# Kernel tuning notes

Hardware: AMD Instinct MI355X
Metric: run time of the kernel (lower is better)

Reference implementation:

```python
import jax, jax.numpy as jnp
import numpy as np
from jax import lax

WS = 8          # window size
HEADS = 8
DIM = 192       # embed_dim == v_dim inside block
HD = DIM // HEADS
SCALE = HD ** -0.5
EPS = 1e-5


def _rel_pos_index(ws):
    coords = np.stack(np.meshgrid(np.arange(ws), np.arange(ws), indexing='ij'))  # (2,ws,ws)
    cf = coords.reshape(2, -1)                       # (2, n)
    rel = (cf[:, :, None] - cf[:, None, :]).transpose(1, 2, 0).astype(np.int64)  # (n,n,2)
    rel[..., 0] += ws - 1
    rel[..., 1] += ws - 1
    rel[..., 0] *= 2 * ws - 1
    return rel.sum(-1)                               # (n, n) int


def _ln(x, w, b):
    m = jnp.mean(x, axis=-1, keepdims=True)
    v = jnp.mean(jnp.square(x - m), axis=-1, keepdims=True)
    return (x - m) * lax.rsqrt(v + EPS) * w + b


def _conv3x3(x, w, b):
    y = lax.conv_general_dilated(x, w, (1, 1), ((1, 1), (1, 1)),
                                 dimension_numbers=('NCHW', 'OIHW', 'NCHW'))
    return y + b[None, :, None, None]


def setup_inputs():
    key = jax.random.key(0)
    ks = jax.random.split(key, 24)
    f = lambda k, shape: (jax.random.normal(k, shape, jnp.float32) * 0.02)
    inp = {
        'x': jax.random.normal(ks[0], (8, 96, 128, 128), jnp.float32),
        'v': jax.random.normal(ks[1], (8, 96, 128, 128), jnp.float32),
        'pq_w': f(ks[2], (DIM, 96, 3, 3)), 'pq_b': f(ks[3], (DIM,)),
        'pv_w': f(ks[4], (DIM, 96, 3, 3)), 'pv_b': f(ks[5], (DIM,)),
        'n1_w': jnp.ones((DIM,)), 'n1_b': jnp.zeros((DIM,)),
        'n2_w': jnp.ones((DIM,)), 'n2_b': jnp.zeros((DIM,)),
        'n3_w': jnp.ones((DIM,)), 'n3_b': jnp.zeros((DIM,)),
        'n4_w': jnp.ones((DIM,)), 'n4_b': jnp.zeros((DIM,)),
        'q_w': f(ks[6], (DIM, DIM)),
        'kv_w': f(ks[7], (2 * DIM, DIM)),
        'ap_w': f(ks[8], (DIM, DIM)), 'ap_b': f(ks[9], (DIM,)),
        'rpb': f(ks[10], ((2 * WS - 1) * (2 * WS - 1), HEADS)),
        'fc1_w': f(ks[11], (4 * DIM, DIM)), 'fc1_b': f(ks[12], (4 * DIM,)),
        'fc2_w': f(ks[13], (DIM, 4 * DIM)), 'fc2_b': f(ks[14], (DIM,)),
    }
    return inp


def reference(x, v, pq_w, pq_b, pv_w, pv_b, n1_w, n1_b, n2_w, n2_b, n3_w, n3_b,
              n4_w, n4_b, q_w, kv_w, ap_w, ap_b, rpb, fc1_w, fc1_b, fc2_w, fc2_b):
    # conv projections (input_dim != embed_dim, v_dim != embed_dim)
    x = _conv3x3(x, pq_w, pq_b)
    v = _conv3x3(v, pv_w, pv_b)
    x_proj, v_proj = x, v
    b, c, h, w = x.shape
    n = WS * WS

    xs = _ln(x.reshape(b, c, h * w).transpose(0, 2, 1), n1_w, n1_b).reshape(b, h, w, c)
    vs = _ln(v.reshape(b, c, h * w).transpose(0, 2, 1), n2_w, n2_b).reshape(b, h, w, c)

    pad_r = (WS - w % WS) % WS
    pad_b_ = (WS - h % WS) % WS
    if pad_r or pad_b_:
        xs = jnp.pad(xs, ((0, 0), (0, pad_b_), (0, pad_r), (0, 0)))
        vs = jnp.pad(vs, ((0, 0), (0, pad_b_), (0, pad_r), (0, 0)))
    hp, wp = h + pad_b_, w + pad_r

    def partition(t):  # (b,hp,wp,c) -> (nw, n, c)
        t = t.reshape(b, hp // WS, WS, wp // WS, WS, c)
        return t.transpose(0, 1, 3, 2, 4, 5).reshape(-1, n, c)

    xw = partition(xs)
    vw = partition(vs)

    # cross-window attention
    q = (xw @ q_w.T).reshape(-1, n, HEADS, HD).transpose(0, 2, 1, 3) * SCALE  # (nw,H,n,hd)
    kv = (vw @ kv_w.T).reshape(-1, n, 2, HEADS, HD).transpose(2, 0, 3, 1, 4)
    k, vv = kv[0], kv[1]                                                     # (nw,H,n,hd)
    attn = jnp.einsum('whqd,whkd->whqk', q, k)
    rel_idx = _rel_pos_index(WS)                                             # static (n,n)
    bias = rpb[rel_idx.reshape(-1)].reshape(n, n, HEADS).transpose(2, 0, 1)  # (H,n,n)
    attn = jax.nn.softmax(attn + bias[None], axis=-1)
    out = jnp.einsum('whqk,whkd->whqd', attn, vv).transpose(0, 2, 1, 3).reshape(-1, n, c)
    out = out @ ap_w.T + ap_b                                                # (nw,n,c)

    # window reverse + crop
    out = out.reshape(b, hp // WS, wp // WS, WS, WS, c).transpose(0, 1, 3, 2, 4, 5)
    out = out.reshape(b, hp, wp, c)[:, :h, :w, :].reshape(b, h * w, c)

    # mlp: note original does x = mlp(norm3(x)); x = x + drop_path(x) -> 2*mlp_out
    m = _ln(out, n3_w, n3_b)
    m = jax.nn.gelu(m @ fc1_w.T + fc1_b, approximate=False) @ fc2_w.T + fc2_b
    m = m + m
    m = _ln(m, n4_w, n4_b)
    m = m.reshape(b, h, w, c).transpose(0, 3, 1, 2)
    return m + x_proj + v_proj
```

## Files before the change

kernel.cpp:

```cpp
#include <hip/hip_runtime.h>
#include <hip/hip_bf16.h>
#include <math.h>

typedef _Float16 f16;
typedef _Float16 half8 __attribute__((ext_vector_type(8)));
typedef float f32x4 __attribute__((ext_vector_type(4)));

#define IMG 128
#define CIN 96
#define CH  192
#define SCALE_Q 0.2041241452319315f

__device__ __forceinline__ f32x4 mfma16(half8 a, half8 b, f32x4 c) {
  return __builtin_amdgcn_mfma_f32_16x16x32_f16(a, b, c, 0, 0, 0);
}

template <bool WH>
__device__ __forceinline__ half8 loadW(const void* W, int row, int k, int ldk) {
  if constexpr (WH) {
    return *(const half8*)((const f16*)W + (size_t)row * ldk + k);
  } else {
    const float* p = (const float*)W + (size_t)row * ldk + k;
    const float4 a = *(const float4*)p;
    const float4 b = *(const float4*)(p + 4);
    half8 h;
    h[0] = (f16)a.x; h[1] = (f16)a.y; h[2] = (f16)a.z; h[3] = (f16)a.w;
    h[4] = (f16)b.x; h[5] = (f16)b.y; h[6] = (f16)b.z; h[7] = (f16)b.w;
    return h;
  }
}

__device__ __forceinline__ float gelu(float x) {
  const float u = 0.70710678118654752f * x;
  const float a = fabsf(u);
  const float t = 1.0f / (1.0f + 0.3275911f * a);
  const float poly = t * (0.254829592f + t * (-0.284496736f +
                     t * (1.421413741f + t * (-1.453152027f + t * 1.061405429f))));
  float er = 1.0f - poly * __expf(-u * u);
  er = (u < 0.f) ? -er : er;
  return 0.5f * x * (1.0f + er);
}

__global__ __launch_bounds__(256) void reorder_w(
    const float* __restrict__ pq_w, const float* __restrict__ pv_w,
    const float* __restrict__ qW, const float* __restrict__ kvW,
    f16* __restrict__ Wr, f16* __restrict__ wq16) {
  const int i = blockIdx.x * 256 + threadIdx.x;
  if (i < 2 * 192 * 864) {
    const int which = i / (192 * 864);
    const int rem = i - which * (192 * 864);
    const int co = rem / 864;
    const int kk = rem - co * 864;
    const int s = kk / 96;
    const int ci = kk - s * 96;
    const float* src = which ? pv_w : pq_w;
    Wr[i] = (f16)src[co * 864 + ci * 9 + s];
  } else if (wq16) {
    const int j = i - 2 * 192 * 864;
    if (j < 110592)
      wq16[j] = (f16)(j < 36864 ? qW[j] : kvW[j - 36864]);
  }
}

__global__ __launch_bounds__(256) void reorder_w2(
    const float* __restrict__ apW, const float* __restrict__ w1,
    const float* __restrict__ w2, f16* __restrict__ dst) {
  const int i = blockIdx.x * 256 + threadIdx.x;
  if (i >= 331776) return;
  float v;
  if (i < 36864)       v = apW[i];
  else if (i < 184320) v = w1[i - 36864];
  else                 v = w2[i - 184320];
  dst[i] = (f16)v;
}

__global__ __launch_bounds__(256, 2) void conv3x3_mfma(
    const float* __restrict__ xin, const float* __restrict__ vin,
    const f16* __restrict__ Wr,
    const float* __restrict__ pq_b, const float* __restrict__ pv_b,
    f16* __restrict__ xp, f16* __restrict__ vp) {
  int bz = blockIdx.x;
  const int which = bz >> 10; bz &= 1023;
  const int b = bz >> 7;
  const int yp = (bz >> 1) & 63;
  const int xseg = bz & 1;
  const int y0 = yp * 2;
  const int x0 = xseg * 64;
  const float* in = which ? vin : xin;
  const float* bias = which ? pv_b : pq_b;
  const f16* W = Wr + (size_t)which * 192 * 864;
  f16* out = which ? vp : xp;

  __shared__ __align__(16) f16 ST[4 * 66 * 104];
  const int tid = threadIdx.x;
  #pragma unroll
  for (int batch = 0; batch < 9; ++batch) {
    float vals[11];
    bool oks[11];
    int sts[11];
    #pragma unroll
    for (int u = 0; u < 11; ++u) {
      const int i = tid + (batch * 11 + u) * 256;
      const int r = i / 6336;
      const int rem2 = i - r * 6336;
      const int c = rem2 / 66;
      const int xx = rem2 - c * 66;
      const int gy = y0 + r - 1;
      const int gx = x0 - 1 + xx;
      oks[u] = ((unsigned)gy < IMG) && ((unsigned)gx < IMG);
      const int cgy = min(max(gy, 0), IMG - 1);
      const int cgx = min(max(gx, 0), IMG - 1);
      vals[u] = in[(((size_t)b * CIN + c) * IMG + cgy) * IMG + cgx];
      sts[u] = (r * 66 + xx) * 104 + c;
    }
    #pragma unroll
    for (int u = 0; u < 11; ++u)
      ST[sts[u]] = oks[u] ? (f16)vals[u] : (f16)0.f;
  }
  __syncthreads();

  const int lane = tid & 63;
  const int wv = tid >> 6;
  const int l15 = lane & 15;
  const int quad = lane >> 4;
  const int nb = wv * 48;

  f32x4 acc[8][3];
  #pragma unroll
  for (int mt = 0; mt < 8; ++mt)
    #pragma unroll
    for (int j = 0; j < 3; ++j) acc[mt][j] = (f32x4)0.f;

  #pragma unroll
  for (int s = 0; s < 9; ++s) {
    const int ky = s / 3, kx = s - ky * 3;
    #pragma unroll
    for (int kstep = 0; kstep < 3; ++kstep) {
      const int k = kstep * 32 + quad * 8;
      half8 a[8];
      #pragma unroll
      for (int mt = 0; mt < 8; ++mt)
        a[mt] = *(const half8*)(ST + (((mt >> 2) + ky) * 66 + (mt & 3) * 16 + l15 + kx) * 104 + k);
      #pragma unroll
      for (int j = 0; j < 3; ++j) {
        const half8 bf = *(const half8*)(W + (size_t)(nb + j * 16 + l15) * 864 + s * 96 + k);
        #pragma unroll
        for (int mt = 0; mt < 8; ++mt) acc[mt][j] = mfma16(a[mt], bf, acc[mt][j]);
      }
    }
  }
  __syncthreads();

  #pragma unroll
  for (int j = 0; j < 3; ++j) {
    const int n = nb + j * 16 + l15;
    const float bn = bias[n];
    #pragma unroll
    for (int mt = 0; mt < 8; ++mt) {
      const int lt = (mt >> 2) * 64 + (mt & 3) * 16 + quad * 4;
      #pragma unroll
      for (int reg = 0; reg < 4; ++reg)
        ST[(lt + reg) * 204 + n] = (f16)(acc[mt][j][reg] + bn);
    }
  }
  __syncthreads();

  const size_t rowbase0 = ((size_t)(b * IMG + y0) * IMG + x0) * CH;
  const size_t rowbase1 = ((size_t)(b * IMG + y0 + 1) * IMG + x0) * CH;
  #pragma unroll
  for (int it = 0; it < 12; ++it) {
    const int i = tid + it * 256;
    const int tok = i / 24, c8 = i - tok * 24;
    const half8 hval = *(const half8*)(ST + tok * 204 + c8 * 8);
    const int trow = tok >> 6, tx = tok & 63;
    f16* dst = out + (trow ? rowbase1 : rowbase0) + (size_t)tx * CH + c8 * 8;
    *(half8*)dst = hval;
  }
}

template <bool WH>
__global__ __launch_bounds__(256, 1) void ln_qkv_mfma(
    f16* __restrict__ xp, const f16* __restrict__ vp,
    const float* __restrict__ n1w, const float* __restrict__ n1b,
    const float* __restrict__ n2w, const float* __restrict__ n2b,
    const void* __restrict__ qW, const void* __restrict__ kvW,
    f16* __restrict__ qb, f16* __restrict__ kb, f16* __restrict__ vb) {
  const int tid = threadIdx.x;
  const int lane = tid & 63;
  const int wv = tid >> 6;
  const int l15 = lane & 15;
  const int quad = lane >> 4;
  const int tok0 = blockIdx.x * 32;
  __shared__ __align__(16) f16 U[32 * 588];
  f16* Ax = U;
  f16* Av = U + 6400;

  {
    const int r = tid >> 3;
    const int s = tid & 7;
    const size_t gbase = (size_t)(tok0 + r) * 192 + s * 24;
    half8 hx[3], hv[3];
    const half8* px = (const half8*)(xp + gbase);
    const half8* pv = (const half8*)(vp + gbase);
    #pragma unroll
    for (int i = 0; i < 3; ++i) { hx[i] = px[i]; hv[i] = pv[i]; }
    float xv[24], vvv[24];
    float sx = 0.f, sx2 = 0.f, sv = 0.f, sv2 = 0.f;
    #pragma unroll
    for (int i = 0; i < 24; ++i) {
      xv[i] = (float)hx[i >> 3][i & 7];
      vvv[i] = (float)hv[i >> 3][i & 7];
      sx += xv[i]; sx2 += xv[i] * xv[i];
      sv += vvv[i]; sv2 += vvv[i] * vvv[i];
    }
    half8 hr[3];
    #pragma unroll
    for (int i = 0; i < 24; ++i) hr[i >> 3][i & 7] = (f16)(xv[i] + vvv[i]);
    half8* pr = (half8*)(xp + gbase);
    #pragma unroll
    for (int i = 0; i < 3; ++i) pr[i] = hr[i];
    #pragma unroll
    for (int m = 1; m < 8; m <<= 1) {
      sx += __shfl_xor(sx, m, 64); sx2 += __shfl_xor(sx2, m, 64);
      sv += __shfl_xor(sv, m, 64); sv2 += __shfl_xor(sv2, m, 64);
    }
    const float mx = sx * (1.f / 192.f);
    const float rx = rsqrtf(sx2 * (1.f / 192.f) - mx * mx + 1e-5f);
    const float mv = sv * (1.f / 192.f);
    const float rv = rsqrtf(sv2 * (1.f / 192.f) - mv * mv + 1e-5f);
    #pragma unroll
    for (int i = 0; i < 24; ++i) {
      const int c = s * 24 + i;
      Ax[r * 200 + c] = (f16)((xv[i] - mx) * rx * n1w[c] + n1b[c]);
      Av[r * 200 + c] = (f16)((vvv[i] - mv) * rv * n2w[c] + n2b[c]);
    }
  }
  __syncthreads();

  const int nb = wv * 144;
  f32x4 acc[2][9];
  #pragma unroll
  for (int mt = 0; mt < 2; ++mt)
    #pragma unroll
    for (int j = 0; j < 9; ++j) acc[mt][j] = (f32x4)0.f;

  for (int kc = 0; kc < 6; ++kc) {
    const int k = kc * 32 + quad * 8;
    half8 wb[9];
    #pragma unroll
    for (int j = 0; j < 9; ++j) {
      const int n0 = nb + j * 16;
      if (n0 < 192) wb[j] = loadW<WH>(qW, n0 + l15, k, 192);
      else          wb[j] = loadW<WH>(kvW, n0 - 192 + l15, k, 192);
    }
    const half8 ax0 = *(const half8*)(Ax + l15 * 200 + k);
    const half8 ax1 = *(const half8*)(Ax + (16 + l15) * 200 + k);
    const half8 av0 = *(const half8*)(Av + l15 * 200 + k);
    const half8 av1 = *(const half8*)(Av + (16 + l15) * 200 + k);
    #pragma unroll
    for (int j = 0; j < 9; ++j) {
      const int n0 = nb + j * 16;
      if (n0 < 192) {
        acc[0][j] = mfma16(ax0, wb[j], acc[0][j]);
        acc[1][j] = mfma16(ax1, wb[j], acc[1][j]);
      } else {
        acc[0][j] = mfma16(av0, wb[j], acc[0][j]);
        acc[1][j] = mfma16(av1, wb[j], acc[1][j]);
      }
    }
  }
  __syncthreads();

  #pragma unroll
  for (int j = 0; j < 9; ++j) {
    const int n = nb + j * 16 + l15;
    const float scale = (n < 192) ? SCALE_Q : 1.f;
    #pragma unroll
    for (int mt = 0; mt < 2; ++mt)
      #pragma unroll
      for (int reg = 0; reg < 4; ++reg) {
        const int r = mt * 16 + quad * 4 + reg;
        U[r * 588 + n] = (f16)(acc[mt][j][reg] * scale);
      }
  }
  __syncthreads();

  const int yrow = (tok0 >> 7) & 127;
  const int bb = tok0 >> 14;
  const int x0b = tok0 & 127;
  const int wib = bb * 256 + ((yrow >> 3) << 4) + (x0b >> 3);
  const int trow = (yrow & 7) * 8;
  f16* const bufs[3] = {qb, kb, vb};
  #pragma unroll
  for (int it = 0; it < 9; ++it) {
    const int i = tid + it * 256;
    const int c24 = i % 24;
    const int g = i / 24;
    const int h = g & 7;
    const int g2 = g >> 3;
    const int wloc = g2 & 3;
    const int buf = g2 >> 2;
    const int t8 = c24 / 3, c3 = c24 - t8 * 3;
    const int r = wloc * 8 + t8;
    const half8 hval = *(const half8*)(U + r * 588 + buf * 192 + h * 24 + c3 * 8);
    f16* dst = bufs[buf] + (size_t)(wib + wloc) * 12288 + (trow + t8) * 24 + h * 1536 + c3 * 8;
    *(half8*)dst = hval;
  }
}

__global__ __launch_bounds__(64) void attn64(
    const f16* __restrict__ qb, const f16* __restrict__ kb,
    const f16* __restrict__ vb, const float* __restrict__ rpb,
    f16* __restrict__ fb) {
  const int wh = blockIdx.x;
  const int h = wh & 7;
  const int w = wh >> 3;
  const int t = threadIdx.x;
  __shared__ __align__(16) float ks[64 * 24];
  __shared__ __align__(16) float vs[64 * 24];
  __shared__ float bsh[225];
  const f16* kbase = kb + (size_t)wh * 1536;
  const f16* vbase = vb + (size_t)wh * 1536;
  for (int i = t; i < 1536; i += 64) { ks[i] = (float)kbase[i]; vs[i] = (float)vbase[i]; }
  for (int i = t; i < 225; i += 64) bsh[i] = rpb[i * 8 + h];
  float q[24];
  const f16* qrow = qb + ((size_t)wh * 64 + t) * 24;
  #pragma unroll
  for (int d = 0; d < 24; ++d) q[d] = (float)qrow[d];
  __syncthreads();
  const int qy = t >> 3, qx = t & 7;
  float s[64];
  float mx = -1e30f;
  #pragma unroll
  for (int kk = 0; kk < 64; ++kk) {
    float acc = 0.f;
    #pragma unroll
    for (int d = 0; d < 24; ++d) acc += q[d] * ks[kk * 24 + d];
    const int ky = kk >> 3, kx = kk & 7;
    acc += bsh[(qy - ky + 7) * 15 + (qx - kx + 7)];
    s[kk] = acc;
    mx = fmaxf(mx, acc);
  }
  float sum = 0.f;
  #pragma unroll
  for (int kk = 0; kk < 64; ++kk) { const float e = __expf(s[kk] - mx); s[kk] = e; sum += e; }
  const float inv = 1.0f / sum;
  float o[24];
  #pragma unroll
  for (int d = 0; d < 24; ++d) o[d] = 0.f;
  #pragma unroll
  for (int kk = 0; kk < 64; ++kk) {
    const float p = s[kk];
    #pragma unroll
    for (int d = 0; d < 24; ++d) o[d] += p * vs[kk * 24 + d];
  }
  f16* orow = fb + ((size_t)w * 64 + t) * 192 + h * 24;
  #pragma unroll
  for (int d = 0; d < 24; ++d) orow[d] = (f16)(o[d] * inv);
}

__global__ __launch_bounds__(256, 1) void ap_ln3_mfma(
    f16* __restrict__ fb, const f16* __restrict__ apW,
    const float* __restrict__ apb,
    const float* __restrict__ n3w, const float* __restrict__ n3b) {
  const int tid = threadIdx.x;
  const int lane = tid & 63;
  const int wv = tid >> 6;
  const int l15 = lane & 15;
  const int quad = lane >> 4;
  const int wt0 = blockIdx.x * 64;
  __shared__ __align__(16) f16 As[64 * 200];
  __shared__ float rs[64], rq[64];
  if (tid < 64) { rs[tid] = 0.f; rq[tid] = 0.f; }
  for (int i = tid; i < 64 * 24; i += 256) {
    const int r = i / 24, s = i - r * 24;
    *(half8*)(As + r * 200 + s * 8) = *(const half8*)(fb + (size_t)(wt0 + r) * 192 + s * 8);
  }
  __syncthreads();

  const int nb = wv * 48;
  f32x4 acc[4][3];
  #pragma unroll
  for (int mt = 0; mt < 4; ++mt)
    #pragma unroll
    for (int j = 0; j < 3; ++j) acc[mt][j] = (f32x4)0.f;

  #pragma unroll
  for (int g = 0; g < 2; ++g) {
    half8 wb[3][3];
    #pragma unroll
    for (int u = 0; u < 3; ++u) {
      const int k = (g * 3 + u) * 32 + quad * 8;
      #pragma unroll
      for (int j = 0; j < 3; ++j)
        wb[u][j] = *(const half8*)(apW + (size_t)(nb + j * 16 + l15) * 192 + k);
    }
    #pragma unroll
    for (int u = 0; u < 3; ++u) {
      const int k = (g * 3 + u) * 32 + quad * 8;
      half8 a[4];
      #pragma unroll
      for (int mt = 0; mt < 4; ++mt)
        a[mt] = *(const half8*)(As + (mt * 16 + l15) * 200 + k);
      #pragma unroll
      for (int j = 0; j < 3; ++j)
        #pragma unroll
        for (int mt = 0; mt < 4; ++mt) acc[mt][j] = mfma16(a[mt], wb[u][j], acc[mt][j]);
    }
  }
  float bias[3];
  #pragma unroll
  for (int j = 0; j < 3; ++j) bias[j] = apb[nb + j * 16 + l15];
  #pragma unroll
  for (int mt = 0; mt < 4; ++mt)
    #pragma unroll
    for (int j = 0; j < 3; ++j)
      #pragma unroll
      for (int reg = 0; reg < 4; ++reg) acc[mt][j][reg] += bias[j];

  float ssum[16], ssq[16];
  #pragma unroll
  for (int mt = 0; mt < 4; ++mt)
    #pragma unroll
    for (int reg = 0; reg < 4; ++reg) {
      const int i = mt * 4 + reg;
      const float a0 = acc[mt][0][reg], a1 = acc[mt][1][reg], a2 = acc[mt][2][reg];
      ssum[i] = a0 + a1 + a2;
      ssq[i] = a0 * a0 + a1 * a1 + a2 * a2;
    }
  #pragma unroll
  for (int m = 1; m < 16; m <<= 1)
    #pragma unroll
    for (int i = 0; i < 16; ++i) {
      ssum[i] += __shfl_xor(ssum[i], m, 64);
      ssq[i] += __shfl_xor(ssq[i], m, 64);
    }
  if (l15 == 0) {
    #pragma unroll
    for (int mt = 0; mt < 4; ++mt)
      #pragma unroll
      for (int reg = 0; reg < 4; ++reg) {
        const int row = mt * 16 + quad * 4 + reg;
        atomicAdd(&rs[row], ssum[mt * 4 + reg]);
        atomicAdd(&rq[row], ssq[mt * 4 + reg]);
      }
  }
  __syncthreads();

  float w3[3], b3[3]; int cc[3];
  #pragma unroll
  for (int j = 0; j < 3; ++j) {
    cc[j] = nb + j * 16 + l15;
    w3[j] = n3w[cc[j]]; b3[j] = n3b[cc[j]];
  }
  #pragma unroll
  for (int mt = 0; mt < 4; ++mt)
    #pragma unroll
    for (int reg = 0; reg < 4; ++reg) {
      const int row = mt * 16 + quad * 4 + reg;
      const float mean = rs[row] * (1.f / 192.f);
      const float rstd = rsqrtf(rq[row] * (1.f / 192.f) - mean * mean + 1e-5f);
      #pragma unroll
      for (int j = 0; j < 3; ++j)
        fb[(size_t)(wt0 + row) * 192 + cc[j]] =
            (f16)((acc[mt][j][reg] - mean) * rstd * w3[j] + b3[j]);
    }
}

__global__ __launch_bounds__(256, 2) void mlp_mfma(
    const f16* __restrict__ m, const f16* __restrict__ w1,
    const float* __restrict__ b1, const f16* __restrict__ w2,
    const float* __restrict__ b2,
    const float* __restrict__ n4w, const float* __restrict__ n4b,
    const f16* __restrict__ res, float* __restrict__ out) {
  const int tid = threadIdx.x;
  const int lane = tid & 63;
  const int wv = tid >> 6;
  const int l15 = lane & 15;
  const int quad = lane >> 4;
  const int wt0 = blockIdx.x * 32;
  __shared__ __align__(16) f16 SB[32 * 776];
  __shared__ float rs[32], rq[32];
  if (tid < 32) { rs[tid] = 0.f; rq[tid] = 0.f; }
  for (int i = tid; i < 32 * 24; i += 256) {
    const int r = i / 24, s = i - r * 24;
    *(half8*)(SB + r * 200 + s * 8) = *(const half8*)(m + (size_t)(wt0 + r) * 192 + s * 8);
  }
  __syncthreads();

  const int nb1 = wv * 192;
  f32x4 acc1[2][12];
  #pragma unroll
  for (int mt = 0; mt < 2; ++mt)
    #pragma unroll
    for (int j = 0; j < 12; ++j) acc1[mt][j] = (f32x4)0.f;
  for (int kc = 0; kc < 6; ++kc) {
    const int k = kc * 32 + quad * 8;
    half8 wb[12];
    #pragma unroll
    for (int j = 0; j < 12; ++j)
      wb[j] = *(const half8*)(w1 + (size_t)(nb1 + j * 16 + l15) * 192 + k);
    const half8 a0 = *(const half8*)(SB + l15 * 200 + k);
    const half8 a1 = *(const half8*)(SB + (16 + l15) * 200 + k);
    #pragma unroll
    for (int j = 0; j < 12; ++j) {
      acc1[0][j] = mfma16(a0, wb[j], acc1[0][j]);
      acc1[1][j] = mfma16(a1, wb[j], acc1[1][j]);
    }
  }
  __syncthreads();
  #pragma unroll
  for (int j = 0; j < 12; ++j) {
    const int n = nb1 + j * 16 + l15;
    const float bj = b1[n];
    #pragma unroll
    for (int mt = 0; mt < 2; ++mt)
      #pragma unroll
      for (int reg = 0; reg < 4; ++reg) {
        const int row = mt * 16 + quad * 4 + reg;
        SB[row * 776 + n] = (f16)gelu(acc1[mt][j][reg] + bj);
      }
  }
  __syncthreads();

  const int nb2 = wv * 48;
  int cc[3];
  #pragma unroll
  for (int j = 0; j < 3; ++j) cc[j] = nb2 + j * 16 + l15;
  const int wi = wt0 >> 6;
  const int t_base = wt0 & 63;
  const int b_img = wi >> 8;
  const int wy = (wi >> 4) & 15;
  const int wx = wi & 15;
  float rr[2][3][4];
  #pragma unroll
  for (int mt = 0; mt < 2; ++mt) {
    const int t0 = t_base + mt * 16 + quad * 4;
    const int y = wy * 8 + (t0 >> 3);
    const int xx0 = wx * 8 + (t0 & 7);
    const size_t tokbase = ((size_t)(b_img * 128 + y)) * 128 + xx0;
    #pragma unroll
    for (int j = 0; j < 3; ++j)
      #pragma unroll
      for (int reg = 0; reg < 4; ++reg)
        rr[mt][j][reg] = (float)res[(tokbase + reg) * 192 + cc[j]];
  }

  f32x4 acc2[2][3];
  #pragma unroll
  for (int mt = 0; mt < 2; ++mt)
    #pragma unroll
    for (int j = 0; j < 3; ++j) acc2[mt][j] = (f32x4)0.f;
  for (int g = 0; g < 6; ++g) {
    half8 wb[4][3];
    #pragma unroll
    for (int u = 0; u < 4; ++u) {
      const int k = (g * 4 + u) * 32 + quad * 8;
      #pragma unroll
      for (int j = 0; j < 3; ++j)
        wb[u][j] = *(const half8*)(w2 + (size_t)(nb2 + j * 16 + l15) * 768 + k);
    }
    #pragma unroll
    for (int u = 0; u < 4; ++u) {
      const int k = (g * 4 + u) * 32 + quad * 8;
      const half8 a0 = *(const half8*)(SB + l15 * 776 + k);
      const half8 a1 = *(const half8*)(SB + (16 + l15) * 776 + k);
      #pragma unroll
      for (int j = 0; j < 3; ++j) {
        acc2[0][j] = mfma16(a0, wb[u][j], acc2[0][j]);
        acc2[1][j] = mfma16(a1, wb[u][j], acc2[1][j]);
      }
    }
  }
  float w4[3], b4[3];
  #pragma unroll
  for (int j = 0; j < 3; ++j) {
    const float bj = b2[cc[j]];
    w4[j] = n4w[cc[j]]; b4[j] = n4b[cc[j]];
    #pragma unroll
    for (int mt = 0; mt < 2; ++mt)
      #pragma unroll
      for (int reg = 0; reg < 4; ++reg)
        acc2[mt][j][reg] = 2.f * (acc2[mt][j][reg] + bj);
  }
  float ssum[8], ssq[8];
  #pragma unroll
  for (int mt = 0; mt < 2; ++mt)
    #pragma unroll
    for (int reg = 0; reg < 4; ++reg) {
      const int i = mt * 4 + reg;
      const float a0 = acc2[mt][0][reg], a1 = acc2[mt][1][reg], a2 = acc2[mt][2][reg];
      ssum[i] = a0 + a1 + a2;
      ssq[i] = a0 * a0 + a1 * a1 + a2 * a2;
    }
  #pragma unroll
  for (int mm = 1; mm < 16; mm <<= 1)
    #pragma unroll
    for (int i = 0; i < 8; ++i) {
      ssum[i] += __shfl_xor(ssum[i], mm, 64);
      ssq[i] += __shfl_xor(ssq[i], mm, 64);
    }
  if (l15 == 0) {
    #pragma unroll
    for (int mt = 0; mt < 2; ++mt)
      #pragma unroll
      for (int reg = 0; reg < 4; ++reg) {
        const int row = mt * 16 + quad * 4 + reg;
        atomicAdd(&rs[row], ssum[mt * 4 + reg]);
        atomicAdd(&rq[row], ssq[mt * 4 + reg]);
      }
  }
  __syncthreads();

  #pragma unroll
  for (int mt = 0; mt < 2; ++mt) {
    const int row0 = mt * 16 + quad * 4;
    const int t0 = t_base + row0;
    const int y = wy * 8 + (t0 >> 3);
    const int x0 = wx * 8 + (t0 & 7);
    float mean[4], rstd[4];
    #pragma unroll
    for (int reg = 0; reg < 4; ++reg) {
      const int row = row0 + reg;
      mean[reg] = rs[row] * (1.f / 192.f);
      rstd[reg] = rsqrtf(rq[row] * (1.f / 192.f) - mean[reg] * mean[reg] + 1e-5f);
    }
    #pragma unroll
    for (int j = 0; j < 3; ++j) {
      float4 o;
      float vals[4];
      #pragma unroll
      for (int reg = 0; reg < 4; ++reg)
        vals[reg] = (acc2[mt][j][reg] - mean[reg]) * rstd[reg] * w4[j] + b4[j] + rr[mt][j][reg];
      o.x = vals[0]; o.y = vals[1]; o.z = vals[2]; o.w = vals[3];
      float* dst = out + ((size_t)(b_img * 192 + cc[j])) * 16384 + (y * 128 + x0);
      *(float4*)dst = o;
    }
  }
}

extern "C" void kernel_launch(void* const* d_in, const int* in_sizes, int n_in,
                              void* d_out, int out_size, void* d_ws, size_t ws_size,
                              hipStream_t stream) {
  (void)in_sizes; (void)n_in; (void)out_size;
  const float* x    = (const float*)d_in[0];
  const float* v    = (const float*)d_in[1];
  const float* pq_w = (const float*)d_in[2];
  const float* pq_b = (const float*)d_in[3];
  const float* pv_w = (const float*)d_in[4];
  const float* pv_b = (const float*)d_in[5];
  const float* n1w  = (const float*)d_in[6];
  const float* n1b  = (const float*)d_in[7];
  const float* n2w  = (const float*)d_in[8];
  const float* n2b  = (const float*)d_in[9];
  const float* n3w  = (const float*)d_in[10];
  const float* n3b  = (const float*)d_in[11];
  const float* n4w  = (const float*)d_in[12];
  const float* n4b  = (const float*)d_in[13];
  const float* qW   = (const float*)d_in[14];
  const float* kvW  = (const float*)d_in[15];
  const float* apW  = (const float*)d_in[16];
  const float* apb  = (const float*)d_in[17];
  const float* rpb  = (const float*)d_in[18];
  const float* w1   = (const float*)d_in[19];
  const float* b1   = (const float*)d_in[20];
  const float* w2   = (const float*)d_in[21];
  const float* b2   = (const float*)d_in[22];
  float* out = (float*)d_out;

  const size_t HE = 25165824;
  f16* xp   = (f16*)d_ws;
  f16* vp   = xp + HE;
  f16* vvb  = vp + HE;
  f16* qb   = (f16*)d_out;
  f16* kb   = qb + HE;
  f16* fb   = vp;
  f16* Wr   = vvb;
  f16* wtail = vvb + HE;
  const bool big = ws_size >= (3 * HE + 110592) * sizeof(f16);

  reorder_w<<<big ? 1728 : 1296, 256, 0, stream>>>(pq_w, pv_w, qW, kvW, Wr,
                                                   big ? wtail : (f16*)nullptr);
  conv3x3_mfma<<<2048, 256, 0, stream>>>(x, v, Wr, pq_b, pv_b, xp, vp);
  if (big)
    ln_qkv_mfma<true><<<4096, 256, 0, stream>>>(xp, vp, n1w, n1b, n2w, n2b,
                                                wtail, wtail + 36864, qb, kb, vvb);
  else
    ln_qkv_mfma<false><<<4096, 256, 0, stream>>>(xp, vp, n1w, n1b, n2w, n2b,
                                                 qW, kvW, qb, kb, vvb);
  attn64<<<16384, 64, 0, stream>>>(qb, kb, vvb, rpb, fb);
  reorder_w2<<<1296, 256, 0, stream>>>(apW, w1, w2, vvb);
  ap_ln3_mfma<<<2048, 256, 0, stream>>>(fb, vvb, apb, n3w, n3b);
  mlp_mfma<<<4096, 256, 0, stream>>>(fb, vvb + 36864, b1, vvb + 184320, b2,
                                     n4w, n4b, xp, out);
}
```

Baseline: 1.050 ms.

## Fuse attention output projection and LayerNorm3 into the MLP kernel

Merges the separate ap_ln3 kernel into the MLP kernel. Each 32-token block now computes the output projection, bias and LN3 in registers and writes the normalized result straight into shared memory for fc1, instead of round-tripping through global memory and paying an extra launch. The MLP kernel now carries extra accumulators and bias registers, which may raise register pressure at two blocks per CU. The GELU reciprocal is also switched to the fast hardware rcp instruction.

```diff
diff --git a/kernel.cpp b/kernel.cpp
--- a/kernel.cpp
+++ b/kernel.cpp
@@ -33,7 +33,7 @@
 __device__ __forceinline__ float gelu(float x) {
   const float u = 0.70710678118654752f * x;
   const float a = fabsf(u);
-  const float t = 1.0f / (1.0f + 0.3275911f * a);
+  const float t = __builtin_amdgcn_rcpf(1.0f + 0.3275911f * a);
   const float poly = t * (0.254829592f + t * (-0.284496736f +
                      t * (1.421413741f + t * (-1.453152027f + t * 1.061405429f))));
   float er = 1.0f - poly * __expf(-u * u);
@@ -359,118 +359,12 @@
   for (int d = 0; d < 24; ++d) orow[d] = (f16)(o[d] * inv);
 }
 
-__global__ __launch_bounds__(256, 1) void ap_ln3_mfma(
-    f16* __restrict__ fb, const f16* __restrict__ apW,
+__global__ __launch_bounds__(256, 2) void ap_mlp_mfma(
+    const f16* __restrict__ fb, const f16* __restrict__ apW,
     const float* __restrict__ apb,
-    const float* __restrict__ n3w, const float* __restrict__ n3b) {
-  const int tid = threadIdx.x;
-  const int lane = tid & 63;
-  const int wv = tid >> 6;
-  const int l15 = lane & 15;
-  const int quad = lane >> 4;
-  const int wt0 = blockIdx.x * 64;
-  __shared__ __align__(16) f16 As[64 * 200];
-  __shared__ float rs[64], rq[64];
-  if (tid < 64) { rs[tid] = 0.f; rq[tid] = 0.f; }
-  for (int i = tid; i < 64 * 24; i += 256) {
-    const int r = i / 24, s = i - r * 24;
-    *(half8*)(As + r * 200 + s * 8) = *(const half8*)(fb + (size_t)(wt0 + r) * 192 + s * 8);
-  }
-  __syncthreads();
-
-  const int nb = wv * 48;
-  f32x4 acc[4][3];
-  #pragma unroll
-  for (int mt = 0; mt < 4; ++mt)
-    #pragma unroll
-    for (int j = 0; j < 3; ++j) acc[mt][j] = (f32x4)0.f;
-
-  #pragma unroll
-  for (int g = 0; g < 2; ++g) {
-    half8 wb[3][3];
-    #pragma unroll
-    for (int u = 0; u < 3; ++u) {
-      const int k = (g * 3 + u) * 32 + quad * 8;
-      #pragma unroll
-      for (int j = 0; j < 3; ++j)
-        wb[u][j] = *(const half8*)(apW + (size_t)(nb + j * 16 + l15) * 192 + k);
-    }
-    #pragma unroll
-    for (int u = 0; u < 3; ++u) {
-      const int k = (g * 3 + u) * 32 + quad * 8;
-      half8 a[4];
-      #pragma unroll
-      for (int mt = 0; mt < 4; ++mt)
-        a[mt] = *(const half8*)(As + (mt * 16 + l15) * 200 + k);
-      #pragma unroll
-      for (int j = 0; j < 3; ++j)
-        #pragma unroll
-        for (int mt = 0; mt < 4; ++mt) acc[mt][j] = mfma16(a[mt], wb[u][j], acc[mt][j]);
-    }
-  }
-  float bias[3];
-  #pragma unroll
-  for (int j = 0; j < 3; ++j) bias[j] = apb[nb + j * 16 + l15];
-  #pragma unroll
-  for (int mt = 0; mt < 4; ++mt)
-    #pragma unroll
-    for (int j = 0; j < 3; ++j)
-      #pragma unroll
-      for (int reg = 0; reg < 4; ++reg) acc[mt][j][reg] += bias[j];
-
-  float ssum[16], ssq[16];
-  #pragma unroll
-  for (int mt = 0; mt < 4; ++mt)
-    #pragma unroll
-    for (int reg = 0; reg < 4; ++reg) {
-      const int i = mt * 4 + reg;
-      const float a0 = acc[mt][0][reg], a1 = acc[mt][1][reg], a2 = acc[mt][2][reg];
-      ssum[i] = a0 + a1 + a2;
-      ssq[i] = a0 * a0 + a1 * a1 + a2 * a2;
-    }
-  #pragma unroll
-  for (int m = 1; m < 16; m <<= 1)
-    #pragma unroll
-    for (int i = 0; i < 16; ++i) {
-      ssum[i] += __shfl_xor(ssum[i], m, 64);
-      ssq[i] += __shfl_xor(ssq[i], m, 64);
-    }
-  if (l15 == 0) {
-    #pragma unroll
-    for (int mt = 0; mt < 4; ++mt)
-      #pragma unroll
-      for (int reg = 0; reg < 4; ++reg) {
-        const int row = mt * 16 + quad * 4 + reg;
-        atomicAdd(&rs[row], ssum[mt * 4 + reg]);
-        atomicAdd(&rq[row], ssq[mt * 4 + reg]);
-      }
-  }
-  __syncthreads();
-
-  float w3[3], b3[3]; int cc[3];
-  #pragma unroll
-  for (int j = 0; j < 3; ++j) {
-    cc[j] = nb + j * 16 + l15;
-    w3[j] = n3w[cc[j]]; b3[j] = n3b[cc[j]];
-  }
-  #pragma unroll
-  for (int mt = 0; mt < 4; ++mt)
-    #pragma unroll
-    for (int reg = 0; reg < 4; ++reg) {
-      const int row = mt * 16 + quad * 4 + reg;
-      const float mean = rs[row] * (1.f / 192.f);
-      const float rstd = rsqrtf(rq[row] * (1.f / 192.f) - mean * mean + 1e-5f);
-      #pragma unroll
-      for (int j = 0; j < 3; ++j)
-        fb[(size_t)(wt0 + row) * 192 + cc[j]] =
-            (f16)((acc[mt][j][reg] - mean) * rstd * w3[j] + b3[j]);
-    }
-}
-
-__global__ __launch_bounds__(256, 2) void mlp_mfma(
-    const f16* __restrict__ m, const f16* __restrict__ w1,
-    const float* __restrict__ b1, const f16* __restrict__ w2,
-    const float* __restrict__ b2,
+    const float* __restrict__ n3w, const float* __restrict__ n3b,
+    const f16* __restrict__ w1, const float* __restrict__ b1,
+    const f16* __restrict__ w2, const float* __restrict__ b2,
     const float* __restrict__ n4w, const float* __restrict__ n4b,
     const f16* __restrict__ res, float* __restrict__ out) {
   const int tid = threadIdx.x;
@@ -480,15 +374,103 @@
   const int quad = lane >> 4;
   const int wt0 = blockIdx.x * 32;
   __shared__ __align__(16) f16 SB[32 * 776];
-  __shared__ float rs[32], rq[32];
-  if (tid < 32) { rs[tid] = 0.f; rq[tid] = 0.f; }
+  __shared__ float rs3[32], rq3[32], rs4[32], rq4[32];
+  if (tid < 32) { rs3[tid] = 0.f; rq3[tid] = 0.f; rs4[tid] = 0.f; rq4[tid] = 0.f; }
   for (int i = tid; i < 32 * 24; i += 256) {
     const int r = i / 24, s = i - r * 24;
-    *(half8*)(SB + r * 200 + s * 8) = *(const half8*)(m + (size_t)(wt0 + r) * 192 + s * 8);
-  }
-  __syncthreads();
-
+    *(half8*)(SB + r * 200 + s * 8) = *(const half8*)(fb + (size_t)(wt0 + r) * 192 + s * 8);
+  }
+  __syncthreads();
+
+  const int nbp = wv * 48;
+  int cc[3]; float apbv[3], w3v[3], b3v[3];
+  #pragma unroll
+  for (int j = 0; j < 3; ++j) {
+    cc[j] = nbp + j * 16 + l15;
+    apbv[j] = apb[cc[j]]; w3v[j] = n3w[cc[j]]; b3v[j] = n3b[cc[j]];
+  }
   const int nb1 = wv * 192;
+  float b1v[12];
+  #pragma unroll
+  for (int j = 0; j < 12; ++j) b1v[j] = b1[nb1 + j * 16 + l15];
+
+  f32x4 accp[2][3];
+  #pragma unroll
+  for (int mt = 0; mt < 2; ++mt)
+    #pragma unroll
+    for (int j = 0; j < 3; ++j) accp[mt][j] = (f32x4)0.f;
+  #pragma unroll
+  for (int g = 0; g < 2; ++g) {
+    half8 wb[3][3];
+    #pragma unroll
+    for (int u = 0; u < 3; ++u) {
+      const int k = (g * 3 + u) * 32 + quad * 8;
+      #pragma unroll
+      for (int j = 0; j < 3; ++j)
+        wb[u][j] = *(const half8*)(apW + (size_t)cc[j] * 192 + k);
+    }
+    #pragma unroll
+    for (int u = 0; u < 3; ++u) {
+      const int k = (g * 3 + u) * 32 + quad * 8;
+      const half8 a0 = *(const half8*)(SB + l15 * 200 + k);
+      const half8 a1 = *(const half8*)(SB + (16 + l15) * 200 + k);
+      #pragma unroll
+      for (int j = 0; j < 3; ++j) {
+        accp[0][j] = mfma16(a0, wb[u][j], accp[0][j]);
+        accp[1][j] = mfma16(a1, wb[u][j], accp[1][j]);
+      }
+    }
+  }
+  #pragma unroll
+  for (int mt = 0; mt < 2; ++mt)
+    #pragma unroll
+    for (int j = 0; j < 3; ++j)
+      #pragma unroll
+      for (int reg = 0; reg < 4; ++reg) accp[mt][j][reg] += apbv[j];
+
+  {
+    float ssum[8], ssq[8];
+    #pragma unroll
+    for (int mt = 0; mt < 2; ++mt)
+      #pragma unroll
+      for (int reg = 0; reg < 4; ++reg) {
+        const int i = mt * 4 + reg;
+        const float a0 = accp[mt][0][reg], a1 = accp[mt][1][reg], a2 = accp[mt][2][reg];
+        ssum[i] = a0 + a1 + a2;
+        ssq[i] = a0 * a0 + a1 * a1 + a2 * a2;
+      }
+    #pragma unroll
+    for (int mm = 1; mm < 16; mm <<= 1)
+      #pragma unroll
+      for (int i = 0; i < 8; ++i) {
+        ssum[i] += __shfl_xor(ssum[i], mm, 64);
+        ssq[i] += __shfl_xor(ssq[i], mm, 64);
+      }
+    if (l15 == 0) {
+      #pragma unroll
+      for (int mt = 0; mt < 2; ++mt)
+        #pragma unroll
+        for (int reg = 0; reg < 4; ++reg) {
+          const int row = mt * 16 + quad * 4 + reg;
+          atomicAdd(&rs3[row], ssum[mt * 4 + reg]);
+          atomicAdd(&rq3[row], ssq[mt * 4 + reg]);
+        }
+    }
+  }
+  __syncthreads();
+  #pragma unroll
+  for (int mt = 0; mt < 2; ++mt)
+    #pragma unroll
+    for (int reg = 0; reg < 4; ++reg) {
+      const int row = mt * 16 + quad * 4 + reg;
+      const float mean = rs3[row] * (1.f / 192.f);
+      const float rstd = rsqrtf(rq3[row] * (1.f / 192.f) - mean * mean + 1e-5f);
+      #pragma unroll
+      for (int j = 0; j < 3; ++j)
+        SB[row * 200 + cc[j]] = (f16)((accp[mt][j][reg] - mean) * rstd * w3v[j] + b3v[j]);
+    }
+  __syncthreads();
+
   f32x4 acc1[2][12];
   #pragma unroll
   for (int mt = 0; mt < 2; ++mt)
@@ -512,21 +494,16 @@
   #pragma unroll
   for (int j = 0; j < 12; ++j) {
     const int n = nb1 + j * 16 + l15;
-    const float bj = b1[n];
     #pragma unroll
     for (int mt = 0; mt < 2; ++mt)
       #pragma unroll
       for (int reg = 0; reg < 4; ++reg) {
         const int row = mt * 16 + quad * 4 + reg;
-        SB[row * 776 + n] = (f16)gelu(acc1[mt][j][reg] + bj);
-      }
-  }
-  __syncthreads();
-
-  const int nb2 = wv * 48;
-  int cc[3];
-  #pragma unroll
-  for (int j = 0; j < 3; ++j) cc[j] = nb2 + j * 16 + l15;
+        SB[row * 776 + n] = (f16)gelu(acc1[mt][j][reg] + b1v[j]);
+      }
+  }
+  __syncthreads();
+
   const int wi = wt0 >> 6;
   const int t_base = wt0 & 63;
   const int b_img = wi >> 8;
@@ -558,7 +535,7 @@
       const int k = (g * 4 + u) * 32 + quad * 8;
       #pragma unroll
       for (int j = 0; j < 3; ++j)
-        wb[u][j] = *(const half8*)(w2 + (size_t)(nb2 + j * 16 + l15) * 768 + k);
+        wb[u][j] = *(const half8*)(w2 + (size_t)cc[j] * 768 + k);
     }
     #pragma unroll
     for (int u = 0; u < 4; ++u) {
@@ -606,8 +583,8 @@
       #pragma unroll
       for (int reg = 0; reg < 4; ++reg) {
         const int row = mt * 16 + quad * 4 + reg;
-        atomicAdd(&rs[row], ssum[mt * 4 + reg]);
-        atomicAdd(&rq[row], ssq[mt * 4 + reg]);
+        atomicAdd(&rs4[row], ssum[mt * 4 + reg]);
+        atomicAdd(&rq4[row], ssq[mt * 4 + reg]);
       }
   }
   __syncthreads();
@@ -622,8 +599,8 @@
     #pragma unroll
     for (int reg = 0; reg < 4; ++reg) {
       const int row = row0 + reg;
-      mean[reg] = rs[row] * (1.f / 192.f);
-      rstd[reg] = rsqrtf(rq[row] * (1.f / 192.f) - mean[reg] * mean[reg] + 1e-5f);
+      mean[reg] = rs4[row] * (1.f / 192.f);
+      rstd[reg] = rsqrtf(rq4[row] * (1.f / 192.f) - mean[reg] * mean[reg] + 1e-5f);
     }
     #pragma unroll
     for (int j = 0; j < 3; ++j) {
@@ -690,7 +667,7 @@
                                                  qW, kvW, qb, kb, vvb);
   attn64<<<16384, 64, 0, stream>>>(qb, kb, vvb, rpb, fb);
   reorder_w2<<<1296, 256, 0, stream>>>(apW, w1, w2, vvb);
-  ap_ln3_mfma<<<2048, 256, 0, stream>>>(fb, vvb, apb, n3w, n3b);
-  mlp_mfma<<<4096, 256, 0, stream>>>(fb, vvb + 36864, b1, vvb + 184320, b2,
-                                     n4w, n4b, xp, out);
-}
+  ap_mlp_mfma<<<4096, 256, 0, stream>>>(fb, vvb, apb, n3w, n3b,
+                                        vvb + 36864, b1, vvb + 184320, b2,
+                                        n4w, n4b, xp, out);
+}
```

Result: no change. 1.031 ms (-1.8%).
